# Kernel tuning notes

Measured on AMD Instinct MI355X. Metric: run time of the kernel, lower is better.

## Reference

```python
import jax, jax.numpy as jnp
import numpy as np

B, T, D, H, L = 1024, 512, 16, 30, 10


def setup_inputs() -> dict:
    key = jax.random.key(0)
    ks = jax.random.split(key, 8)
    s = 1.0 / np.sqrt(H)  # PyTorch RNN init scale (uniform +-1/sqrt(H)); normal*s is fine for a numeric baseline
    return {
        "x": jax.random.normal(ks[0], (B, T, D), dtype=jnp.float32),
        "W_ih0": jax.random.normal(ks[1], (H, D), dtype=jnp.float32) * s,
        "W_ih": jax.random.normal(ks[2], (L - 1, H, H), dtype=jnp.float32) * s,
        "W_hh": jax.random.normal(ks[3], (L, H, H), dtype=jnp.float32) * s,
        "b_ih": jax.random.normal(ks[4], (L, H), dtype=jnp.float32) * s,
        "b_hh": jax.random.normal(ks[5], (L, H), dtype=jnp.float32) * s,
        "fc_w": jax.random.normal(ks[6], (1, H), dtype=jnp.float32) * s,
        "fc_b": jax.random.normal(ks[7], (1,), dtype=jnp.float32) * s,
    }


def _rnn_layer(x, Wi, Wh, bi, bh):
    # x: [B, T, Din] -> [B, T, H]; h_t = tanh(x_t Wi^T + bi + h_{t-1} Wh^T + bh)
    xw = jnp.einsum("btd,hd->bth", x, Wi) + (bi + bh)  # fold both biases once
    h0 = jnp.zeros((x.shape[0], Wh.shape[0]), dtype=x.dtype)

    def step(h, xw_t):
        h = jnp.tanh(xw_t + h @ Wh.T)
        return h, h

    _, ys = jax.lax.scan(step, h0, jnp.swapaxes(xw, 0, 1))  # scan over time
    return jnp.swapaxes(ys, 0, 1)


def reference(x, W_ih0, W_ih, W_hh, b_ih, b_hh, fc_w, fc_b):
    out = _rnn_layer(x, W_ih0, W_hh[0], b_ih[0], b_hh[0])
    for l in range(1, L):
        out = _rnn_layer(out, W_ih[l - 1], W_hh[l], b_ih[l], b_hh[l])
    # fc on last timestep: [B, H] @ [H, 1] + b -> [B, 1]
    return out[:, -1, :] @ fc_w.T + fc_b
```

## Files before the change

### kernel.cpp

```cpp
#include <hip/hip_runtime.h>

#define TT 512
#define DD 16
#define HH 30
#define LL 10
#define C  4
#define TCH (TT / C)
#define RING 3
#define WRH 40
#define GRP 16
#define BLOCKT (LL * 64)
#define KPRE 2.885390081777927f

typedef _Float16 f16x8 __attribute__((ext_vector_type(8)));
typedef float    f32x4 __attribute__((ext_vector_type(4)));

union U128 { uint4 u; f16x8 h; };

#define LINKOFF(l, sl, cc) ((((l) * RING + (sl)) * C + (cc)) * (GRP * WRH))

__device__ __forceinline__ _Float16 tanh_e(float d) {
    const float e = __builtin_amdgcn_exp2f(d);
    return (_Float16)(1.0f - 2.0f * __builtin_amdgcn_rcpf(e + 1.0f));
}

__device__ __forceinline__ int nu_of(int k) {
    return 16 * ((k >> 2) & 1) + 4 * (k >> 3) + (k & 3);
}

__device__ __forceinline__ void wait_ge(unsigned* f, unsigned tgt) {
    while (__hip_atomic_load(f, __ATOMIC_ACQUIRE,
                             __HIP_MEMORY_SCOPE_WORKGROUP) < tgt)
        __builtin_amdgcn_s_sleep(1);
}

__global__ __launch_bounds__(BLOCKT) void rnn_flow(
    const float* __restrict__ x,   const float* __restrict__ wi0,
    const float* __restrict__ wih, const float* __restrict__ whh,
    const float* __restrict__ bih, const float* __restrict__ bhh,
    const float* __restrict__ fcw, const float* __restrict__ fcb,
    float* __restrict__ out)
{
    extern __shared__ __align__(16) _Float16 link[];
    __shared__ unsigned flg[2 * LL];

    const int tid  = threadIdx.x;
    const int l    = tid >> 6;
    const int lane = tid & 63;
    const int n    = lane & 15;
    const int qq   = lane >> 4;
    const int b0   = blockIdx.x * GRP;

    f16x8 wain[2], waown[2];
    #pragma unroll
    for (int tile = 0; tile < 2; ++tile) {
        const int j = 16 * tile + n;
        #pragma unroll
        for (int i = 0; i < 8; ++i) {
            const int kap = 8 * qq + i;
            const int nu  = nu_of(kap);
            float vi = 0.f, vo = 0.f;
            if (j < HH) {
                if (l == 0) { if (kap < DD) vi = wi0[j * DD + kap]; }
                else        { if (nu  < HH) vi = wih[(l - 1) * 900 + j * HH + nu]; }
                if (nu < HH) vo = whh[l * 900 + j * HH + nu];
            }
            wain[tile][i]  = (_Float16)(vi * KPRE);
            waown[tile][i] = (_Float16)(vo * KPRE);
        }
    }
    f32x4 cb[2];
    #pragma unroll
    for (int tile = 0; tile < 2; ++tile)
        #pragma unroll
        for (int r = 0; r < 4; ++r) {
            const int j2 = 16 * tile + 4 * qq + r;
            cb[tile][r] = (j2 < HH) ? (bih[l * HH + j2] + bhh[l * HH + j2]) * KPRE : 0.f;
        }
    float fcl[8];
    #pragma unroll
    for (int i = 0; i < 8; ++i) {
        const int nu = nu_of(8 * qq + i);
        fcl[i] = (nu < HH) ? fcw[nu] : 0.f;
    }
    const float fbv = fcb[0];

    float4 xb[C][2];
    const float4* x4 = (const float4*)x;
    const size_t xbase = (size_t)(b0 + n) * TT * 4;
    if (l == 0 && qq < 2) {
        #pragma unroll
        for (int cc = 0; cc < C; ++cc) {
            xb[cc][0] = x4[xbase + cc * 4 + 2 * qq];
            xb[cc][1] = x4[xbase + cc * 4 + 2 * qq + 1];
        }
    }

    f16x8 bown;
    #pragma unroll
    for (int i = 0; i < 8; ++i) bown[i] = (_Float16)0.f;

    if (tid < 2 * LL) flg[tid] = 0u;
    __syncthreads();

    unsigned sl = 0;
    for (int pt = 0; pt < TCH; ++pt) {
        U128 binu[C];
        if (l == 0) {
            #pragma unroll
            for (int cc = 0; cc < C; ++cc) {
                if (qq < 2) {
                    const float4 u = xb[cc][0], v = xb[cc][1];
                    binu[cc].h[0] = (_Float16)u.x; binu[cc].h[1] = (_Float16)u.y;
                    binu[cc].h[2] = (_Float16)u.z; binu[cc].h[3] = (_Float16)u.w;
                    binu[cc].h[4] = (_Float16)v.x; binu[cc].h[5] = (_Float16)v.y;
                    binu[cc].h[6] = (_Float16)v.z; binu[cc].h[7] = (_Float16)v.w;
                    if (pt + 1 < TCH) {
                        const int tn = (pt + 1) * C + cc;
                        xb[cc][0] = x4[xbase + tn * 4 + 2 * qq];
                        xb[cc][1] = x4[xbase + tn * 4 + 2 * qq + 1];
                    }
                } else {
                    binu[cc].u = uint4{0u, 0u, 0u, 0u};
                }
            }
        } else {
            wait_ge(&flg[l - 1], (unsigned)(pt + 1));
            #pragma unroll
            for (int cc = 0; cc < C; ++cc)
                binu[cc].u = *(const uint4*)(link + LINKOFF(l - 1, sl, cc)
                                             + n * WRH + 8 * qq);
        }

        f32x4 dp0[C], dp1[C];
        #pragma unroll
        for (int cc = 0; cc < C; ++cc) {
            dp0[cc] = __builtin_amdgcn_mfma_f32_16x16x32_f16(wain[0], binu[cc].h, cb[0], 0, 0, 0);
            dp1[cc] = __builtin_amdgcn_mfma_f32_16x16x32_f16(wain[1], binu[cc].h, cb[1], 0, 0, 0);
        }
        if (l > 0 && lane == 0)
            __hip_atomic_store(&flg[LL + l], (unsigned)(pt + 1),
                               __ATOMIC_RELEASE, __HIP_MEMORY_SCOPE_WORKGROUP);

        if (l < LL - 1 && pt >= RING)
            wait_ge(&flg[LL + l + 1], (unsigned)(pt - RING + 1));

        #pragma unroll
        for (int cc = 0; cc < C; ++cc) {
            const f32x4 d0 = __builtin_amdgcn_mfma_f32_16x16x32_f16(waown[0], bown, dp0[cc], 0, 0, 0);
            const f32x4 d1 = __builtin_amdgcn_mfma_f32_16x16x32_f16(waown[1], bown, dp1[cc], 0, 0, 0);
            f16x8 nb;
            #pragma unroll
            for (int r = 0; r < 4; ++r) {
                nb[r]     = tanh_e(d0[r]);
                nb[4 + r] = tanh_e(d1[r]);
            }
            bown = nb;
            if (l < LL - 1) {
                U128 uu; uu.h = nb;
                *(uint4*)(link + LINKOFF(l, sl, cc) + n * WRH + 8 * qq) = uu.u;
            }
        }
        if (l < LL - 1 && lane == 0)
            __hip_atomic_store(&flg[l], (unsigned)(pt + 1),
                               __ATOMIC_RELEASE, __HIP_MEMORY_SCOPE_WORKGROUP);

        sl = (sl == RING - 1) ? 0u : sl + 1u;
    }

    if (l == LL - 1) {
        float v = 0.f;
        #pragma unroll
        for (int i = 0; i < 8; ++i) v = fmaf((float)bown[i], fcl[i], v);
        v += __shfl_xor(v, 16);
        v += __shfl_xor(v, 32);
        if (qq == 0) out[b0 + n] = v + fbv;
    }
}

extern "C" void kernel_launch(void* const* d_in, const int* in_sizes, int n_in,
                              void* d_out, int out_size, void* d_ws, size_t ws_size,
                              hipStream_t stream) {
    const float* x   = (const float*)d_in[0];
    const float* wi0 = (const float*)d_in[1];
    const float* wih = (const float*)d_in[2];
    const float* whh = (const float*)d_in[3];
    const float* bih = (const float*)d_in[4];
    const float* bhh = (const float*)d_in[5];
    const float* fcw = (const float*)d_in[6];
    const float* fcb = (const float*)d_in[7];
    float* out = (float*)d_out;

    const size_t lds_bytes =
        (size_t)((LL - 1) * RING * C * GRP * WRH) * sizeof(_Float16);
    hipFuncSetAttribute((const void*)rnn_flow,
                        hipFuncAttributeMaxDynamicSharedMemorySize,
                        (int)lds_bytes);

    rnn_flow<<<1024 / GRP, BLOCKT, lds_bytes, stream>>>(x, wi0, wih, whh,
                                                        bih, bhh, fcw, fcb, out);
}
```

Baseline: 225.4 us.

## Carry sigmoid-form hidden state to drop tanh affine ops; unroll ring slots

The kernel rewrites tanh(z) as 1-2*sigmoid(2z) and carries s=sigmoid instead of h. The -2 factor goes into the weights and the row sums go into the biases and the fc offset, which removes the per-element 1-2*r step from the serial recurrence. It also uses packed cvt_pkrtz conversions, a contiguous per-lane LDS link layout, and a fully unrolled RING of 4 so slot offsets become compile-time constants. The risk is a small precision change, since fp16 now stores values near 0.5 and biases absorb summed weights.

```diff
diff --git a/kernel.cpp b/kernel.cpp
--- a/kernel.cpp
+++ b/kernel.cpp
@@ -6,22 +6,24 @@
 #define LL 10
 #define C  4
 #define TCH (TT / C)
-#define RING 3
-#define WRH 40
+#define RING 4
 #define GRP 16
 #define BLOCKT (LL * 64)
 #define KPRE 2.885390081777927f
 
+#define CC_H   512
+#define SL_H   (C * CC_H)
+#define LINK_H (RING * SL_H)
+
 typedef _Float16 f16x8 __attribute__((ext_vector_type(8)));
+typedef _Float16 h2    __attribute__((ext_vector_type(2)));
 typedef float    f32x4 __attribute__((ext_vector_type(4)));
 
-union U128 { uint4 u; f16x8 h; };
-
-#define LINKOFF(l, sl, cc) ((((l) * RING + (sl)) * C + (cc)) * (GRP * WRH))
-
-__device__ __forceinline__ _Float16 tanh_e(float d) {
+union U128 { uint4 u; f16x8 h; h2 p[4]; };
+
+__device__ __forceinline__ float sigma_e(float d) {
     const float e = __builtin_amdgcn_exp2f(d);
-    return (_Float16)(1.0f - 2.0f * __builtin_amdgcn_rcpf(e + 1.0f));
+    return __builtin_amdgcn_rcpf(e + 1.0f);
 }
 
 __device__ __forceinline__ int nu_of(int k) {
@@ -34,7 +36,7 @@
         __builtin_amdgcn_s_sleep(1);
 }
 
-__global__ __launch_bounds__(BLOCKT) void rnn_flow(
+__global__ __launch_bounds__(BLOCKT) void rnn_sig(
     const float* __restrict__ x,   const float* __restrict__ wi0,
     const float* __restrict__ wih, const float* __restrict__ whh,
     const float* __restrict__ bih, const float* __restrict__ bhh,
@@ -61,9 +63,9 @@
             const int nu  = nu_of(kap);
             float vi = 0.f, vo = 0.f;
             if (j < HH) {
-                if (l == 0) { if (kap < DD) vi = wi0[j * DD + kap]; }
-                else        { if (nu  < HH) vi = wih[(l - 1) * 900 + j * HH + nu]; }
-                if (nu < HH) vo = whh[l * 900 + j * HH + nu];
+                if (l == 0) { if (kap < DD) vi =  wi0[j * DD + kap]; }
+                else        { if (nu  < HH) vi = -2.f * wih[(l - 1) * 900 + j * HH + nu]; }
+                if (nu < HH) vo = -2.f * whh[l * 900 + j * HH + nu];
             }
             wain[tile][i]  = (_Float16)(vi * KPRE);
             waown[tile][i] = (_Float16)(vo * KPRE);
@@ -75,15 +77,23 @@
         #pragma unroll
         for (int r = 0; r < 4; ++r) {
             const int j2 = 16 * tile + 4 * qq + r;
-            cb[tile][r] = (j2 < HH) ? (bih[l * HH + j2] + bhh[l * HH + j2]) * KPRE : 0.f;
+            float v = 0.f;
+            if (j2 < HH) {
+                v = bih[l * HH + j2] + bhh[l * HH + j2];
+                for (int k = 0; k < HH; ++k) v += whh[l * 900 + j2 * HH + k];
+                if (l > 0)
+                    for (int k = 0; k < HH; ++k) v += wih[(l - 1) * 900 + j2 * HH + k];
+            }
+            cb[tile][r] = v * KPRE;
         }
     float fcl[8];
     #pragma unroll
     for (int i = 0; i < 8; ++i) {
         const int nu = nu_of(8 * qq + i);
-        fcl[i] = (nu < HH) ? fcw[nu] : 0.f;
-    }
-    const float fbv = fcb[0];
+        fcl[i] = (nu < HH) ? -2.f * fcw[nu] : 0.f;
+    }
+    float fbv = fcb[0];
+    for (int k = 0; k < HH; ++k) fbv += fcw[k];
 
     float4 xb[C][2];
     const float4* x4 = (const float4*)x;
@@ -96,76 +106,76 @@
         }
     }
 
+    _Float16* lin_r = link + (l - 1) * LINK_H + lane * 8;
+    _Float16* lin_w = link + l * LINK_H + lane * 8;
+
     f16x8 bown;
     #pragma unroll
-    for (int i = 0; i < 8; ++i) bown[i] = (_Float16)0.f;
+    for (int i = 0; i < 8; ++i) bown[i] = (_Float16)0.5f;
 
     if (tid < 2 * LL) flg[tid] = 0u;
     __syncthreads();
 
-    unsigned sl = 0;
-    for (int pt = 0; pt < TCH; ++pt) {
-        U128 binu[C];
-        if (l == 0) {
+    for (int pb = 0; pb < TCH; pb += RING) {
+        #pragma unroll
+        for (int sl = 0; sl < RING; ++sl) {
+            const int pt = pb + sl;
+
+            U128 binu[C];
+            if (l == 0) {
+                #pragma unroll
+                for (int cc = 0; cc < C; ++cc) {
+                    if (qq < 2) {
+                        const float4 u = xb[cc][0], v = xb[cc][1];
+                        binu[cc].p[0] = (h2)__builtin_amdgcn_cvt_pkrtz(u.x, u.y);
+                        binu[cc].p[1] = (h2)__builtin_amdgcn_cvt_pkrtz(u.z, u.w);
+                        binu[cc].p[2] = (h2)__builtin_amdgcn_cvt_pkrtz(v.x, v.y);
+                        binu[cc].p[3] = (h2)__builtin_amdgcn_cvt_pkrtz(v.z, v.w);
+                        if (pt + 1 < TCH) {
+                            const int tn = (pt + 1) * C + cc;
+                            xb[cc][0] = x4[xbase + tn * 4 + 2 * qq];
+                            xb[cc][1] = x4[xbase + tn * 4 + 2 * qq + 1];
+                        }
+                    } else {
+                        binu[cc].u = uint4{0u, 0u, 0u, 0u};
+                    }
+                }
+            } else {
+                wait_ge(&flg[l - 1], (unsigned)(pt + 1));
+                #pragma unroll
+                for (int cc = 0; cc < C; ++cc)
+                    binu[cc].u = *(const uint4*)(lin_r + sl * SL_H + cc * CC_H);
+            }
+
+            f32x4 dp0[C], dp1[C];
             #pragma unroll
             for (int cc = 0; cc < C; ++cc) {
-                if (qq < 2) {
-                    const float4 u = xb[cc][0], v = xb[cc][1];
-                    binu[cc].h[0] = (_Float16)u.x; binu[cc].h[1] = (_Float16)u.y;
-                    binu[cc].h[2] = (_Float16)u.z; binu[cc].h[3] = (_Float16)u.w;
-                    binu[cc].h[4] = (_Float16)v.x; binu[cc].h[5] = (_Float16)v.y;
-                    binu[cc].h[6] = (_Float16)v.z; binu[cc].h[7] = (_Float16)v.w;
-                    if (pt + 1 < TCH) {
-                        const int tn = (pt + 1) * C + cc;
-                        xb[cc][0] = x4[xbase + tn * 4 + 2 * qq];
-                        xb[cc][1] = x4[xbase + tn * 4 + 2 * qq + 1];
-                    }
-                } else {
-                    binu[cc].u = uint4{0u, 0u, 0u, 0u};
-                }
-            }
-        } else {
-            wait_ge(&flg[l - 1], (unsigned)(pt + 1));
+                dp0[cc] = __builtin_amdgcn_mfma_f32_16x16x32_f16(wain[0], binu[cc].h, cb[0], 0, 0, 0);
+                dp1[cc] = __builtin_amdgcn_mfma_f32_16x16x32_f16(wain[1], binu[cc].h, cb[1], 0, 0, 0);
+            }
+            if (l > 0 && lane == 0)
+                __hip_atomic_store(&flg[LL + l], (unsigned)(pt + 1),
+                                   __ATOMIC_RELEASE, __HIP_MEMORY_SCOPE_WORKGROUP);
+            if (l < LL - 1 && pt >= RING)
+                wait_ge(&flg[LL + l + 1], (unsigned)(pt - RING + 1));
+
             #pragma unroll
-            for (int cc = 0; cc < C; ++cc)
-                binu[cc].u = *(const uint4*)(link + LINKOFF(l - 1, sl, cc)
-                                             + n * WRH + 8 * qq);
-        }
-
-        f32x4 dp0[C], dp1[C];
-        #pragma unroll
-        for (int cc = 0; cc < C; ++cc) {
-            dp0[cc] = __builtin_amdgcn_mfma_f32_16x16x32_f16(wain[0], binu[cc].h, cb[0], 0, 0, 0);
-            dp1[cc] = __builtin_amdgcn_mfma_f32_16x16x32_f16(wain[1], binu[cc].h, cb[1], 0, 0, 0);
-        }
-        if (l > 0 && lane == 0)
-            __hip_atomic_store(&flg[LL + l], (unsigned)(pt + 1),
-                               __ATOMIC_RELEASE, __HIP_MEMORY_SCOPE_WORKGROUP);
-
-        if (l < LL - 1 && pt >= RING)
-            wait_ge(&flg[LL + l + 1], (unsigned)(pt - RING + 1));
-
-        #pragma unroll
-        for (int cc = 0; cc < C; ++cc) {
-            const f32x4 d0 = __builtin_amdgcn_mfma_f32_16x16x32_f16(waown[0], bown, dp0[cc], 0, 0, 0);
-            const f32x4 d1 = __builtin_amdgcn_mfma_f32_16x16x32_f16(waown[1], bown, dp1[cc], 0, 0, 0);
-            f16x8 nb;
-            #pragma unroll
-            for (int r = 0; r < 4; ++r) {
-                nb[r]     = tanh_e(d0[r]);
-                nb[4 + r] = tanh_e(d1[r]);
-            }
-            bown = nb;
-            if (l < LL - 1) {
-                U128 uu; uu.h = nb;
-                *(uint4*)(link + LINKOFF(l, sl, cc) + n * WRH + 8 * qq) = uu.u;
-            }
-        }
-        if (l < LL - 1 && lane == 0)
-            __hip_atomic_store(&flg[l], (unsigned)(pt + 1),
-                               __ATOMIC_RELEASE, __HIP_MEMORY_SCOPE_WORKGROUP);
-
-        sl = (sl == RING - 1) ? 0u : sl + 1u;
+            for (int cc = 0; cc < C; ++cc) {
+                const f32x4 d0 = __builtin_amdgcn_mfma_f32_16x16x32_f16(waown[0], bown, dp0[cc], 0, 0, 0);
+                const f32x4 d1 = __builtin_amdgcn_mfma_f32_16x16x32_f16(waown[1], bown, dp1[cc], 0, 0, 0);
+                U128 uu;
+                uu.p[0] = (h2)__builtin_amdgcn_cvt_pkrtz(sigma_e(d0[0]), sigma_e(d0[1]));
+                uu.p[1] = (h2)__builtin_amdgcn_cvt_pkrtz(sigma_e(d0[2]), sigma_e(d0[3]));
+                uu.p[2] = (h2)__builtin_amdgcn_cvt_pkrtz(sigma_e(d1[0]), sigma_e(d1[1]));
+                uu.p[3] = (h2)__builtin_amdgcn_cvt_pkrtz(sigma_e(d1[2]), sigma_e(d1[3]));
+                bown = uu.h;
+                if (l < LL - 1)
+                    *(uint4*)(lin_w + sl * SL_H + cc * CC_H) = uu.u;
+            }
+            if (l < LL - 1 && lane == 0)
+                __hip_atomic_store(&flg[l], (unsigned)(pt + 1),
+                                   __ATOMIC_RELEASE, __HIP_MEMORY_SCOPE_WORKGROUP);
+        }
     }
 
     if (l == LL - 1) {
@@ -191,12 +201,11 @@
     const float* fcb = (const float*)d_in[7];
     float* out = (float*)d_out;
 
-    const size_t lds_bytes =
-        (size_t)((LL - 1) * RING * C * GRP * WRH) * sizeof(_Float16);
-    hipFuncSetAttribute((const void*)rnn_flow,
+    const size_t lds_bytes = (size_t)(LL - 1) * LINK_H * sizeof(_Float16);
+    hipFuncSetAttribute((const void*)rnn_sig,
                         hipFuncAttributeMaxDynamicSharedMemorySize,
                         (int)lds_bytes);
 
-    rnn_flow<<<1024 / GRP, BLOCKT, lds_bytes, stream>>>(x, wi0, wih, whh,
-                                                        bih, bhh, fcw, fcb, out);
-}
+    rnn_sig<<<1024 / GRP, BLOCKT, lds_bytes, stream>>>(x, wi0, wih, whh,
+                                                       bih, bhh, fcw, fcb, out);
+}
```

New measurement: 204.4 us. 1.1x faster.
